# Kernel optimization log

Hardware: AMD Instinct MI355X
Metric: run time of the kernel (lower is better)

Reference implementation:

```python
import jax, jax.numpy as jnp
import numpy as np

D_MODEL = 1024
NUM_HEADS = 16
D_K = D_MODEL // NUM_HEADS
BATCH = 2
SEQ = 2048


def setup_inputs() -> dict:
    key = jax.random.key(0)
    ks = jax.random.split(key, 9)
    s = 1.0 / np.sqrt(D_MODEL)
    X = jax.random.normal(ks[0], (BATCH, SEQ, D_MODEL), dtype=jnp.float32)
    # causal mask, broadcastable over batch and heads; 0 means masked
    mask = jnp.tril(jnp.ones((SEQ, SEQ), dtype=jnp.int32))[None, None]
    W_Q = jax.random.uniform(ks[1], (D_MODEL, D_MODEL), jnp.float32, -s, s)
    b_Q = jax.random.uniform(ks[2], (D_MODEL,), jnp.float32, -s, s)
    W_K = jax.random.uniform(ks[3], (D_MODEL, D_MODEL), jnp.float32, -s, s)
    b_K = jax.random.uniform(ks[4], (D_MODEL,), jnp.float32, -s, s)
    W_V = jax.random.uniform(ks[5], (D_MODEL, D_MODEL), jnp.float32, -s, s)
    b_V = jax.random.uniform(ks[6], (D_MODEL,), jnp.float32, -s, s)
    W_O = jax.random.uniform(ks[7], (D_MODEL, D_MODEL), jnp.float32, -s, s)
    b_O = jax.random.uniform(ks[8], (D_MODEL,), jnp.float32, -s, s)
    return {"X": X, "mask": mask, "W_Q": W_Q, "b_Q": b_Q, "W_K": W_K,
            "b_K": b_K, "W_V": W_V, "b_V": b_V, "W_O": W_O, "b_O": b_O}


def reference(X, mask, W_Q, b_Q, W_K, b_K, W_V, b_V, W_O, b_O):
    B, S, _ = X.shape
    H, Dk = NUM_HEADS, D_K
    # projections; torch Linear uses y = x @ W.T + b; here W_* is stored as [in, out]
    Q = (X @ W_Q + b_Q).reshape(B, S, H, Dk).transpose(0, 2, 1, 3)  # [B,H,S,Dk]
    K = (X @ W_K + b_K).reshape(B, S, H, Dk).transpose(0, 2, 1, 3)
    V = (X @ W_V + b_V).reshape(B, S, H, Dk).transpose(0, 2, 1, 3)
    scores = jnp.einsum("bhqd,bhkd->bhqk", Q, K) / jnp.sqrt(jnp.asarray(Dk, X.dtype))
    scores = jnp.where(mask == 0, -jnp.inf, scores)
    attn = jax.nn.softmax(scores, axis=-1)  # [B,H,S,S]
    out = jnp.einsum("bhqk,bhkd->bhqd", attn, V)
    out = out.transpose(0, 2, 1, 3).reshape(B, S, H * Dk)
    return out @ W_O + b_O
```

## Files before the change

### kernel.cpp

```cpp
#include <hip/hip_runtime.h>
#include <math.h>

#define S_LEN 2048
#define DM 1024
#define NH 16
#define DK 64
#define BB 2
#define MROWS (BB * S_LEN)
#define QTILES (S_LEN / 64)
#define LOG2E 1.44269504088896340736f

typedef __attribute__((ext_vector_type(8))) short bf16x8;
typedef __attribute__((ext_vector_type(4))) float f32x4;

__device__ __forceinline__ unsigned short f2bf(float f) {
    unsigned int u = __builtin_bit_cast(unsigned int, f);
    u += 0x7fff + ((u >> 16) & 1);
    return (unsigned short)(u >> 16);
}

__device__ __forceinline__ float hw_exp2(float x) {
    return __builtin_amdgcn_exp2f(x);
}

__device__ __forceinline__ void gload_lds16(const unsigned short* g, unsigned short* l) {
    __builtin_amdgcn_global_load_lds(
        (const __attribute__((address_space(1))) unsigned int*)(const void*)g,
        (__attribute__((address_space(3))) unsigned int*)(void*)l, 16, 0, 0);
}

__global__ __launch_bounds__(256) void prep_kernel(
    const float* __restrict__ X, unsigned short* __restrict__ Xb,
    const float* __restrict__ W_Q, const float* __restrict__ W_K,
    const float* __restrict__ W_V, const float* __restrict__ W_O,
    unsigned short* __restrict__ WqkvT, unsigned short* __restrict__ WoT) {
    const int z = blockIdx.z;
    if (z == 0) {
        int i = (blockIdx.x * 256 + threadIdx.x) * 4;
        float4 v = *(const float4*)(X + i);
        ushort4 o;
        o.x = f2bf(v.x); o.y = f2bf(v.y); o.z = f2bf(v.z); o.w = f2bf(v.w);
        *(ushort4*)(Xb + i) = o;
        return;
    }
    if (blockIdx.x >= (DM / 32) * (DM / 32)) return;
    const float* in = z == 1 ? W_Q : (z == 2 ? W_K : (z == 3 ? W_V : W_O));
    unsigned short* out = z == 4 ? WoT : (WqkvT + (size_t)(z - 1) * DM * DM);
    __shared__ float tile[32][33];
    const int bx = blockIdx.x & 31, by = blockIdx.x >> 5;
    const int tx = threadIdx.x & 31, ty = threadIdx.x >> 5;
    const int c = bx * 32 + tx;
#pragma unroll
    for (int i = 0; i < 32; i += 8)
        tile[ty + i][tx] = in[(size_t)(by * 32 + ty + i) * DM + c];
    __syncthreads();
    const int oc = by * 32 + tx;
#pragma unroll
    for (int i = 0; i < 32; i += 8)
        out[(size_t)(bx * 32 + ty + i) * DM + oc] = f2bf(tile[tx][ty + i]);
}

__global__ __launch_bounds__(256) void gemm_qkv_kernel(
    const unsigned short* __restrict__ A,
    const unsigned short* __restrict__ Bt,
    const float* __restrict__ bQ, const float* __restrict__ bK,
    const float* __restrict__ bV,
    unsigned short* __restrict__ outQ, unsigned short* __restrict__ outK,
    unsigned short* __restrict__ outV) {
    const int K = DM;
    __shared__ __align__(16) unsigned short smem[4 * 64 * 72];
    const int tid = threadIdx.x;
    const int wave = tid >> 6, lane = tid & 63;
    const int lq = lane >> 4, ln = lane & 15;
    const int m0 = blockIdx.y * 128, n0 = blockIdx.x * 128;
    const int wr = (wave >> 1) * 64, wc = (wave & 1) * 64;

    f32x4 acc[4][4];
#pragma unroll
    for (int i = 0; i < 4; ++i)
#pragma unroll
        for (int j = 0; j < 4; ++j)
            acc[i][j] = (f32x4){0.f, 0.f, 0.f, 0.f};

    const unsigned short* ga = A  + (size_t)(m0 + (tid >> 2)) * K + (tid & 3) * 8;
    const unsigned short* gb = Bt + (size_t)(n0 + (tid >> 2)) * K + (tid & 3) * 8;
    const size_t half = (size_t)64 * K;

    {
        unsigned short* An = smem;
        unsigned short* Bn = smem + 4096;
        gload_lds16(ga, An + tid * 8);
        gload_lds16(ga + half, An + 2048 + tid * 8);
        gload_lds16(gb, Bn + tid * 8);
        gload_lds16(gb + half, Bn + 2048 + tid * 8);
    }

    for (int k0 = 0; k0 < K; k0 += 32) {
        const int cur = (k0 >> 5) & 1;
        unsigned short* As = smem + cur * 8192;
        unsigned short* Bs = As + 4096;
        __syncthreads();
        if (k0 + 32 < K) {
            unsigned short* An = smem + (cur ^ 1) * 8192;
            unsigned short* Bn = An + 4096;
            gload_lds16(ga + k0 + 32, An + tid * 8);
            gload_lds16(ga + half + k0 + 32, An + 2048 + tid * 8);
            gload_lds16(gb + k0 + 32, Bn + tid * 8);
            gload_lds16(gb + half + k0 + 32, Bn + 2048 + tid * 8);
        }
        bf16x8 af[4], bfv[4];
#pragma unroll
        for (int i = 0; i < 4; ++i) af[i]  = *(const bf16x8*)&As[(wr + i * 16 + ln) * 32 + lq * 8];
#pragma unroll
        for (int j = 0; j < 4; ++j) bfv[j] = *(const bf16x8*)&Bs[(wc + j * 16 + ln) * 32 + lq * 8];
#pragma unroll
        for (int i = 0; i < 4; ++i)
#pragma unroll
            for (int j = 0; j < 4; ++j)
                acc[i][j] = __builtin_amdgcn_mfma_f32_16x16x32_bf16(af[i], bfv[j], acc[i][j], 0, 0, 0);
    }
    __syncthreads();

    const int which = n0 >> 10;
    const float* bias = which == 0 ? bQ : (which == 1 ? bK : bV);
    const float scale = which == 0 ? 0.125f * LOG2E : 1.0f;
    unsigned short* ob = which == 0 ? outQ : (which == 1 ? outK : outV);
    unsigned short* Ts = &smem[wave * 64 * 72];
#pragma unroll
    for (int i = 0; i < 4; ++i)
#pragma unroll
        for (int j = 0; j < 4; ++j)
#pragma unroll
            for (int r = 0; r < 4; ++r) {
                int rl = i * 16 + lq * 4 + r;
                int cl = j * 16 + ln;
                float v = (acc[i][j][r] + bias[(n0 & 1023) + wc + cl]) * scale;
                if (which == 2) Ts[cl * 72 + rl] = f2bf(v);
                else            Ts[rl * 72 + cl] = f2bf(v);
            }
    const int hh = ((n0 & 1023) + wc) >> 6;
    const int bI = (m0 + wr) >> 11, sbase = (m0 + wr) & 2047;
    if (which <= 1) {
        unsigned short* dst = ob + ((size_t)(bI * NH + hh) * S_LEN + sbase) * DK;
#pragma unroll
        for (int t = 0; t < 8; ++t) {
            int rl = t * 8 + (lane >> 3);
            *(uint4*)(dst + rl * DK + (lane & 7) * 8) =
                *(const uint4*)&Ts[rl * 72 + (lane & 7) * 8];
        }
    } else {
        unsigned short* dst = ob + ((size_t)(bI * NH + hh) * DK) * S_LEN + sbase;
#pragma unroll
        for (int t = 0; t < 8; ++t) {
            int dkl = t * 8 + (lane >> 3);
            *(uint4*)(dst + (size_t)dkl * S_LEN + (lane & 7) * 8) =
                *(const uint4*)&Ts[dkl * 72 + (lane & 7) * 8];
        }
    }
}

__global__ __launch_bounds__(256) void gemm_o_kernel(
    const unsigned short* __restrict__ A,
    const unsigned short* __restrict__ Bt,
    const float* __restrict__ bias,
    float* __restrict__ out_f) {
    const int K = DM;
    __shared__ __align__(16) unsigned short smem[2 * 6144];
    const int tid = threadIdx.x;
    const int wave = tid >> 6, lane = tid & 63;
    const int lq = lane >> 4, ln = lane & 15;
    const int m0 = blockIdx.y * 128, n0 = blockIdx.x * 64;
    const int wr = (wave >> 1) * 64, wc = (wave & 1) * 32;

    f32x4 acc[4][2];
#pragma unroll
    for (int i = 0; i < 4; ++i)
#pragma unroll
        for (int j = 0; j < 2; ++j)
            acc[i][j] = (f32x4){0.f, 0.f, 0.f, 0.f};

    const unsigned short* ga = A  + (size_t)(m0 + (tid >> 2)) * K + (tid & 3) * 8;
    const unsigned short* gb = Bt + (size_t)(n0 + (tid >> 2)) * K + (tid & 3) * 8;
    const size_t half = (size_t)64 * K;

    {
        unsigned short* An = smem;
        gload_lds16(ga, An + tid * 8);
        gload_lds16(ga + half, An + 2048 + tid * 8);
        gload_lds16(gb, An + 4096 + tid * 8);
    }

    for (int k0 = 0; k0 < K; k0 += 32) {
        const int cur = (k0 >> 5) & 1;
        unsigned short* As = smem + cur * 6144;
        unsigned short* Bs = As + 4096;
        __syncthreads();
        if (k0 + 32 < K) {
            unsigned short* An = smem + (cur ^ 1) * 6144;
            gload_lds16(ga + k0 + 32, An + tid * 8);
            gload_lds16(ga + half + k0 + 32, An + 2048 + tid * 8);
            gload_lds16(gb + k0 + 32, An + 4096 + tid * 8);
        }
        bf16x8 af[4], bfv[2];
#pragma unroll
        for (int i = 0; i < 4; ++i) af[i]  = *(const bf16x8*)&As[(wr + i * 16 + ln) * 32 + lq * 8];
#pragma unroll
        for (int j = 0; j < 2; ++j) bfv[j] = *(const bf16x8*)&Bs[(wc + j * 16 + ln) * 32 + lq * 8];
#pragma unroll
        for (int i = 0; i < 4; ++i)
#pragma unroll
            for (int j = 0; j < 2; ++j)
                acc[i][j] = __builtin_amdgcn_mfma_f32_16x16x32_bf16(af[i], bfv[j], acc[i][j], 0, 0, 0);
    }

#pragma unroll
    for (int i = 0; i < 4; ++i)
#pragma unroll
        for (int j = 0; j < 2; ++j)
#pragma unroll
            for (int r = 0; r < 4; ++r) {
                int m = m0 + wr + i * 16 + lq * 4 + r;
                int n = n0 + wc + j * 16 + ln;
                out_f[(size_t)m * DM + n] = acc[i][j][r] + bias[n];
            }
}

__global__ __launch_bounds__(256, 2) void attn_kernel(
    const unsigned short* __restrict__ Qg,
    const unsigned short* __restrict__ Kg,
    const unsigned short* __restrict__ Vg,
    unsigned short* __restrict__ Og) {
    __shared__ __align__(16) unsigned short KBUF[2 * 128 * 64];
    __shared__ __align__(16) unsigned short VBUF[2 * 64 * 128];
    __shared__ __align__(16) unsigned short Pw[4 * 2 * 640];

    const int tid = threadIdx.x;
    const int wave = tid >> 6, lane = tid & 63;
    const int lq = lane >> 4, ln = lane & 15;
    const int bh = blockIdx.x, b = bh >> 4, h = bh & 15;
    const int bx = blockIdx.y;
    const int qtA = QTILES - 1 - bx, qtB = bx;
    const int nkvA = (qtA + 2) >> 1;
    const int nkvB = (qtB + 2) >> 1;
    const int T = nkvA + nkvB;

    const unsigned short* Qb = Qg + (size_t)bh * S_LEN * DK;
    const unsigned short* Kb = Kg + (size_t)bh * S_LEN * DK;
    const unsigned short* Vb = Vg + (size_t)bh * DK * S_LEN;

    const int krow_l = lane >> 3;
    const int kchunk = (lane & 7) ^ krow_l;
    const int vrow_l = lane >> 4;

    {
#pragma unroll
        for (int s = 0; s < 4; ++s)
            gload_lds16(Kb + (size_t)(wave * 32 + s * 8 + krow_l) * DK + kchunk * 8,
                        KBUF + (wave * 32 + s * 8) * 64 + lane * 8);
#pragma unroll
        for (int s = 0; s < 4; ++s) {
            int rv = wave * 16 + s * 4 + vrow_l;
            int c  = (lane & 15) ^ (s * 4 + vrow_l);
            gload_lds16(Vb + (size_t)rv * S_LEN + c * 8,
                        VBUF + (wave * 16 + s * 4) * 128 + lane * 8);
        }
    }

    int q0 = qtA * 64;
    const int qrowoff = wave * 16 + ln;
    bf16x8 qf0 = *(const bf16x8*)(Qb + (q0 + qrowoff) * DK + lq * 8);
    bf16x8 qf1 = *(const bf16x8*)(Qb + (q0 + qrowoff) * DK + 32 + lq * 8);

    const short one_bf = (short)0x3F80;
    const bf16x8 onesf = {one_bf, one_bf, one_bf, one_bf,
                          one_bf, one_bf, one_bf, one_bf};

    f32x4 oacc[4];
    f32x4 lacc = (f32x4){0.f, 0.f, 0.f, 0.f};
#pragma unroll
    for (int i = 0; i < 4; ++i) oacc[i] = (f32x4){0.f, 0.f, 0.f, 0.f};
    float m0r = -INFINITY, m1r = -INFINITY, m2r = -INFINITY, m3r = -INFINITY;

    for (int g = 0; g < T; ++g) {
        const int cur = g & 1;
        unsigned short* Kl = KBUF + cur * 8192;
        unsigned short* Vl = VBUF + cur * 8192;
        __syncthreads();

        if (g + 1 < T) {
            const int kv0n = (g + 1 < nkvA ? g + 1 : g + 1 - nkvA) * 128;
            unsigned short* Kn = KBUF + (cur ^ 1) * 8192;
            unsigned short* Vn = VBUF + (cur ^ 1) * 8192;
#pragma unroll
            for (int s = 0; s < 4; ++s)
                gload_lds16(Kb + (size_t)(kv0n + wave * 32 + s * 8 + krow_l) * DK + kchunk * 8,
                            Kn + (wave * 32 + s * 8) * 64 + lane * 8);
#pragma unroll
            for (int s = 0; s < 4; ++s) {
                int rv = wave * 16 + s * 4 + vrow_l;
                int c  = (lane & 15) ^ (s * 4 + vrow_l);
                gload_lds16(Vb + (size_t)rv * S_LEN + kv0n + c * 8,
                            Vn + (wave * 16 + s * 4) * 128 + lane * 8);
            }
        }

        const int kv0 = (g < nkvA ? g : g - nkvA) * 128;
        const bool lastOfSeg = (g == nkvA - 1) || (g == T - 1);

        f32x4 sc[8];
#pragma unroll
        for (int ct = 0; ct < 8; ++ct) {
            const int rbase = (ct * 16 + ln) * 64;
            bf16x8 k0 = *(const bf16x8*)&Kl[rbase + ((lq ^ (ln & 7)) * 8)];
            bf16x8 k1 = *(const bf16x8*)&Kl[rbase + (((lq + 4) ^ (ln & 7)) * 8)];
            f32x4 a = (f32x4){0.f, 0.f, 0.f, 0.f};
            a = __builtin_amdgcn_mfma_f32_16x16x32_bf16(qf0, k0, a, 0, 0, 0);
            a = __builtin_amdgcn_mfma_f32_16x16x32_bf16(qf1, k1, a, 0, 0, 0);
            sc[ct] = a;
        }

        if (lastOfSeg) {
#pragma unroll
            for (int ct = 0; ct < 8; ++ct) {
                int col = kv0 + ct * 16 + ln;
#pragma unroll
                for (int r = 0; r < 4; ++r) {
                    int row = q0 + wave * 16 + lq * 4 + r;
                    if (col > row) sc[ct][r] = -INFINITY;
                }
            }
        }

#pragma unroll
        for (int r = 0; r < 4; ++r) {
            float mx = fmaxf(fmaxf(fmaxf(sc[0][r], sc[1][r]), fmaxf(sc[2][r], sc[3][r])),
                             fmaxf(fmaxf(sc[4][r], sc[5][r]), fmaxf(sc[6][r], sc[7][r])));
#pragma unroll
            for (int off = 1; off < 16; off <<= 1)
                mx = fmaxf(mx, __shfl_xor(mx, off));
            float mold = r == 0 ? m0r : (r == 1 ? m1r : (r == 2 ? m2r : m3r));
            float mnew = fmaxf(mold, mx);
            float alpha = hw_exp2(mold - mnew);
#pragma unroll
            for (int dkt = 0; dkt < 4; ++dkt) oacc[dkt][r] *= alpha;
            lacc[r] *= alpha;
#pragma unroll
            for (int ct = 0; ct < 8; ++ct)
                sc[ct][r] = hw_exp2(sc[ct][r] - mnew);
            if (r == 0) m0r = mnew;
            else if (r == 1) m1r = mnew;
            else if (r == 2) m2r = mnew;
            else m3r = mnew;
        }

        unsigned short* Pp0 = Pw + wave * 1280;
#pragma unroll
        for (int qd = 0; qd < 4; ++qd) {
            unsigned short* Pq = Pp0 + (qd & 1) * 640;
#pragma unroll
            for (int c2 = 0; c2 < 2; ++c2)
#pragma unroll
                for (int r = 0; r < 4; ++r)
                    Pq[(lq * 4 + r) * 40 + c2 * 16 + ln] = f2bf(sc[qd * 2 + c2][r]);
            bf16x8 pf = *(const bf16x8*)&Pq[ln * 40 + lq * 8];
            lacc = __builtin_amdgcn_mfma_f32_16x16x32_bf16(pf, onesf, lacc, 0, 0, 0);
#pragma unroll
            for (int dkt = 0; dkt < 4; ++dkt) {
                const unsigned short* vr =
                    &Vl[(dkt * 16 + ln) * 128 + (((qd * 4 + lq) ^ ln) * 8)];
                oacc[dkt] = __builtin_amdgcn_mfma_f32_16x16x32_bf16(pf, *(const bf16x8*)vr, oacc[dkt], 0, 0, 0);
            }
        }

        if (g == nkvA - 1) {
#pragma unroll
            for (int r = 0; r < 4; ++r) {
                float inv = 1.0f / lacc[r];
                int s = q0 + wave * 16 + lq * 4 + r;
#pragma unroll
                for (int dkt = 0; dkt < 4; ++dkt)
                    Og[((size_t)(b * S_LEN + s)) * DM + h * 64 + dkt * 16 + ln] =
                        f2bf(oacc[dkt][r] * inv);
            }
            q0 = qtB * 64;
            qf0 = *(const bf16x8*)(Qb + (q0 + qrowoff) * DK + lq * 8);
            qf1 = *(const bf16x8*)(Qb + (q0 + qrowoff) * DK + 32 + lq * 8);
#pragma unroll
            for (int i = 0; i < 4; ++i) oacc[i] = (f32x4){0.f, 0.f, 0.f, 0.f};
            lacc = (f32x4){0.f, 0.f, 0.f, 0.f};
            m0r = m1r = m2r = m3r = -INFINITY;
        }
    }

#pragma unroll
    for (int r = 0; r < 4; ++r) {
        float inv = 1.0f / lacc[r];
        int s = q0 + wave * 16 + lq * 4 + r;
#pragma unroll
        for (int dkt = 0; dkt < 4; ++dkt)
            Og[((size_t)(b * S_LEN + s)) * DM + h * 64 + dkt * 16 + ln] =
                f2bf(oacc[dkt][r] * inv);
    }
}

extern "C" void kernel_launch(void* const* d_in, const int* in_sizes, int n_in,
                              void* d_out, int out_size, void* d_ws, size_t ws_size,
                              hipStream_t stream) {
    const float* X   = (const float*)d_in[0];
    const float* W_Q = (const float*)d_in[2];
    const float* b_Q = (const float*)d_in[3];
    const float* W_K = (const float*)d_in[4];
    const float* b_K = (const float*)d_in[5];
    const float* W_V = (const float*)d_in[6];
    const float* b_V = (const float*)d_in[7];
    const float* W_O = (const float*)d_in[8];
    const float* b_O = (const float*)d_in[9];

    unsigned short* Xb    = (unsigned short*)d_ws;
    unsigned short* WqkvT = Xb    + (size_t)MROWS * DM;
    unsigned short* WoT   = WqkvT + (size_t)3 * DM * DM;
    unsigned short* Qb    = WoT   + (size_t)DM * DM;
    unsigned short* Kb    = Qb    + (size_t)MROWS * DM;
    unsigned short* Vtb   = Kb    + (size_t)MROWS * DM;
    unsigned short* Ob    = Vtb   + (size_t)MROWS * DM;

    prep_kernel<<<dim3((MROWS * DM) / 1024, 1, 5), 256, 0, stream>>>(
        X, Xb, W_Q, W_K, W_V, W_O, WqkvT, WoT);

    gemm_qkv_kernel<<<dim3(3 * DM / 128, MROWS / 128), 256, 0, stream>>>(
        Xb, WqkvT, b_Q, b_K, b_V, Qb, Kb, Vtb);

    attn_kernel<<<dim3(BB * NH, QTILES / 2), 256, 0, stream>>>(Qb, Kb, Vtb, Ob);

    gemm_o_kernel<<<dim3(DM / 64, MROWS / 128), 256, 0, stream>>>(
        Ob, WoT, b_O, (float*)d_out);
}
```

Before: 197.0 us.

## Process paired causal query tiles concurrently with two wave groups sharing KV tiles

The attention block grows from 256 to 512 threads, and its two wave groups handle the long and short query tiles of a causal pair at the same time. Before, one group handled them one after the other. Both groups share a single stream of double-buffered K/V tiles in LDS, so each KV tile is loaded once per block rather than once per segment. The short-tile group idles once its causal range is done, and the larger block with launch bounds of 4 blocks/CU may squeeze registers or occupancy.

```diff
diff --git a/kernel.cpp b/kernel.cpp
--- a/kernel.cpp
+++ b/kernel.cpp
@@ -225,24 +225,24 @@
             }
 }
 
-__global__ __launch_bounds__(256, 2) void attn_kernel(
+__global__ __launch_bounds__(512, 4) void attn_kernel(
     const unsigned short* __restrict__ Qg,
     const unsigned short* __restrict__ Kg,
     const unsigned short* __restrict__ Vg,
     unsigned short* __restrict__ Og) {
     __shared__ __align__(16) unsigned short KBUF[2 * 128 * 64];
     __shared__ __align__(16) unsigned short VBUF[2 * 64 * 128];
-    __shared__ __align__(16) unsigned short Pw[4 * 2 * 640];
+    __shared__ __align__(16) unsigned short Pw[8 * 640];
 
     const int tid = threadIdx.x;
     const int wave = tid >> 6, lane = tid & 63;
     const int lq = lane >> 4, ln = lane & 15;
     const int bh = blockIdx.x, b = bh >> 4, h = bh & 15;
-    const int bx = blockIdx.y;
-    const int qtA = QTILES - 1 - bx, qtB = bx;
-    const int nkvA = (qtA + 2) >> 1;
-    const int nkvB = (qtB + 2) >> 1;
-    const int T = nkvA + nkvB;
+    const int j = blockIdx.y;
+    const int grp = wave >> 2, wv = wave & 3;
+    const int qt = grp == 0 ? (QTILES - 1 - j) : j;
+    const int nkv_me = grp == 0 ? ((33 - j) >> 1) : ((j + 2) >> 1);
+    const int T = (33 - j) >> 1;
 
     const unsigned short* Qb = Qg + (size_t)bh * S_LEN * DK;
     const unsigned short* Kb = Kg + (size_t)bh * S_LEN * DK;
@@ -254,22 +254,21 @@
 
     {
 #pragma unroll
-        for (int s = 0; s < 4; ++s)
-            gload_lds16(Kb + (size_t)(wave * 32 + s * 8 + krow_l) * DK + kchunk * 8,
-                        KBUF + (wave * 32 + s * 8) * 64 + lane * 8);
-#pragma unroll
-        for (int s = 0; s < 4; ++s) {
-            int rv = wave * 16 + s * 4 + vrow_l;
-            int c  = (lane & 15) ^ (s * 4 + vrow_l);
+        for (int s = 0; s < 2; ++s)
+            gload_lds16(Kb + (size_t)(wave * 16 + s * 8 + krow_l) * DK + kchunk * 8,
+                        KBUF + (wave * 16 + s * 8) * 64 + lane * 8);
+#pragma unroll
+        for (int s = 0; s < 2; ++s) {
+            int rv = wave * 8 + s * 4 + vrow_l;
+            int c  = (lane & 15) ^ (rv & 15);
             gload_lds16(Vb + (size_t)rv * S_LEN + c * 8,
-                        VBUF + (wave * 16 + s * 4) * 128 + lane * 8);
-        }
-    }
-
-    int q0 = qtA * 64;
-    const int qrowoff = wave * 16 + ln;
-    bf16x8 qf0 = *(const bf16x8*)(Qb + (q0 + qrowoff) * DK + lq * 8);
-    bf16x8 qf1 = *(const bf16x8*)(Qb + (q0 + qrowoff) * DK + 32 + lq * 8);
+                        VBUF + (wave * 8 + s * 4) * 128 + lane * 8);
+        }
+    }
+
+    const int q0 = qt * 64;
+    bf16x8 qf0 = *(const bf16x8*)(Qb + (q0 + wv * 16 + ln) * DK + lq * 8);
+    bf16x8 qf1 = *(const bf16x8*)(Qb + (q0 + wv * 16 + ln) * DK + 32 + lq * 8);
 
     const short one_bf = (short)0x3F80;
     const bf16x8 onesf = {one_bf, one_bf, one_bf, one_bf,
@@ -288,114 +287,95 @@
         __syncthreads();
 
         if (g + 1 < T) {
-            const int kv0n = (g + 1 < nkvA ? g + 1 : g + 1 - nkvA) * 128;
+            const int kv0n = (g + 1) * 128;
             unsigned short* Kn = KBUF + (cur ^ 1) * 8192;
             unsigned short* Vn = VBUF + (cur ^ 1) * 8192;
 #pragma unroll
-            for (int s = 0; s < 4; ++s)
-                gload_lds16(Kb + (size_t)(kv0n + wave * 32 + s * 8 + krow_l) * DK + kchunk * 8,
-                            Kn + (wave * 32 + s * 8) * 64 + lane * 8);
-#pragma unroll
-            for (int s = 0; s < 4; ++s) {
-                int rv = wave * 16 + s * 4 + vrow_l;
-                int c  = (lane & 15) ^ (s * 4 + vrow_l);
+            for (int s = 0; s < 2; ++s)
+                gload_lds16(Kb + (size_t)(kv0n + wave * 16 + s * 8 + krow_l) * DK + kchunk * 8,
+                            Kn + (wave * 16 + s * 8) * 64 + lane * 8);
+#pragma unroll
+            for (int s = 0; s < 2; ++s) {
+                int rv = wave * 8 + s * 4 + vrow_l;
+                int c  = (lane & 15) ^ (rv & 15);
                 gload_lds16(Vb + (size_t)rv * S_LEN + kv0n + c * 8,
-                            Vn + (wave * 16 + s * 4) * 128 + lane * 8);
-            }
-        }
-
-        const int kv0 = (g < nkvA ? g : g - nkvA) * 128;
-        const bool lastOfSeg = (g == nkvA - 1) || (g == T - 1);
-
-        f32x4 sc[8];
-#pragma unroll
-        for (int ct = 0; ct < 8; ++ct) {
-            const int rbase = (ct * 16 + ln) * 64;
-            bf16x8 k0 = *(const bf16x8*)&Kl[rbase + ((lq ^ (ln & 7)) * 8)];
-            bf16x8 k1 = *(const bf16x8*)&Kl[rbase + (((lq + 4) ^ (ln & 7)) * 8)];
-            f32x4 a = (f32x4){0.f, 0.f, 0.f, 0.f};
-            a = __builtin_amdgcn_mfma_f32_16x16x32_bf16(qf0, k0, a, 0, 0, 0);
-            a = __builtin_amdgcn_mfma_f32_16x16x32_bf16(qf1, k1, a, 0, 0, 0);
-            sc[ct] = a;
-        }
-
-        if (lastOfSeg) {
+                            Vn + (wave * 8 + s * 4) * 128 + lane * 8);
+            }
+        }
+
+        if (g < nkv_me) {
+            const int kv0 = g * 128;
+
+            f32x4 sc[8];
 #pragma unroll
             for (int ct = 0; ct < 8; ++ct) {
-                int col = kv0 + ct * 16 + ln;
-#pragma unroll
-                for (int r = 0; r < 4; ++r) {
-                    int row = q0 + wave * 16 + lq * 4 + r;
-                    if (col > row) sc[ct][r] = -INFINITY;
+                const int rbase = (ct * 16 + ln) * 64;
+                bf16x8 k0 = *(const bf16x8*)&Kl[rbase + ((lq ^ (ln & 7)) * 8)];
+                bf16x8 k1 = *(const bf16x8*)&Kl[rbase + (((lq + 4) ^ (ln & 7)) * 8)];
+                f32x4 a = (f32x4){0.f, 0.f, 0.f, 0.f};
+                a = __builtin_amdgcn_mfma_f32_16x16x32_bf16(qf0, k0, a, 0, 0, 0);
+                a = __builtin_amdgcn_mfma_f32_16x16x32_bf16(qf1, k1, a, 0, 0, 0);
+                sc[ct] = a;
+            }
+
+            if (g == nkv_me - 1) {
+#pragma unroll
+                for (int ct = 0; ct < 8; ++ct) {
+                    int col = kv0 + ct * 16 + ln;
+#pragma unroll
+                    for (int r = 0; r < 4; ++r) {
+                        int row = q0 + wv * 16 + lq * 4 + r;
+                        if (col > row) sc[ct][r] = -INFINITY;
+                    }
                 }
             }
-        }
-
-#pragma unroll
-        for (int r = 0; r < 4; ++r) {
-            float mx = fmaxf(fmaxf(fmaxf(sc[0][r], sc[1][r]), fmaxf(sc[2][r], sc[3][r])),
-                             fmaxf(fmaxf(sc[4][r], sc[5][r]), fmaxf(sc[6][r], sc[7][r])));
-#pragma unroll
-            for (int off = 1; off < 16; off <<= 1)
-                mx = fmaxf(mx, __shfl_xor(mx, off));
-            float mold = r == 0 ? m0r : (r == 1 ? m1r : (r == 2 ? m2r : m3r));
-            float mnew = fmaxf(mold, mx);
-            float alpha = hw_exp2(mold - mnew);
-#pragma unroll
-            for (int dkt = 0; dkt < 4; ++dkt) oacc[dkt][r] *= alpha;
-            lacc[r] *= alpha;
-#pragma unroll
-            for (int ct = 0; ct < 8; ++ct)
-                sc[ct][r] = hw_exp2(sc[ct][r] - mnew);
-            if (r == 0) m0r = mnew;
-            else if (r == 1) m1r = mnew;
-            else if (r == 2) m2r = mnew;
-            else m3r = mnew;
-        }
-
-        unsigned short* Pp0 = Pw + wave * 1280;
-#pragma unroll
-        for (int qd = 0; qd < 4; ++qd) {
-            unsigned short* Pq = Pp0 + (qd & 1) * 640;
-#pragma unroll
-            for (int c2 = 0; c2 < 2; ++c2)
-#pragma unroll
-                for (int r = 0; r < 4; ++r)
-                    Pq[(lq * 4 + r) * 40 + c2 * 16 + ln] = f2bf(sc[qd * 2 + c2][r]);
-            bf16x8 pf = *(const bf16x8*)&Pq[ln * 40 + lq * 8];
-            lacc = __builtin_amdgcn_mfma_f32_16x16x32_bf16(pf, onesf, lacc, 0, 0, 0);
-#pragma unroll
-            for (int dkt = 0; dkt < 4; ++dkt) {
-                const unsigned short* vr =
-                    &Vl[(dkt * 16 + ln) * 128 + (((qd * 4 + lq) ^ ln) * 8)];
-                oacc[dkt] = __builtin_amdgcn_mfma_f32_16x16x32_bf16(pf, *(const bf16x8*)vr, oacc[dkt], 0, 0, 0);
-            }
-        }
-
-        if (g == nkvA - 1) {
+
 #pragma unroll
             for (int r = 0; r < 4; ++r) {
-                float inv = 1.0f / lacc[r];
-                int s = q0 + wave * 16 + lq * 4 + r;
-#pragma unroll
-                for (int dkt = 0; dkt < 4; ++dkt)
-                    Og[((size_t)(b * S_LEN + s)) * DM + h * 64 + dkt * 16 + ln] =
-                        f2bf(oacc[dkt][r] * inv);
-            }
-            q0 = qtB * 64;
-            qf0 = *(const bf16x8*)(Qb + (q0 + qrowoff) * DK + lq * 8);
-            qf1 = *(const bf16x8*)(Qb + (q0 + qrowoff) * DK + 32 + lq * 8);
-#pragma unroll
-            for (int i = 0; i < 4; ++i) oacc[i] = (f32x4){0.f, 0.f, 0.f, 0.f};
-            lacc = (f32x4){0.f, 0.f, 0.f, 0.f};
-            m0r = m1r = m2r = m3r = -INFINITY;
+                float mx = fmaxf(fmaxf(fmaxf(sc[0][r], sc[1][r]), fmaxf(sc[2][r], sc[3][r])),
+                                 fmaxf(fmaxf(sc[4][r], sc[5][r]), fmaxf(sc[6][r], sc[7][r])));
+#pragma unroll
+                for (int off = 1; off < 16; off <<= 1)
+                    mx = fmaxf(mx, __shfl_xor(mx, off));
+                float mold = r == 0 ? m0r : (r == 1 ? m1r : (r == 2 ? m2r : m3r));
+                float mnew = fmaxf(mold, mx);
+                float alpha = hw_exp2(mold - mnew);
+#pragma unroll
+                for (int dkt = 0; dkt < 4; ++dkt) oacc[dkt][r] *= alpha;
+                lacc[r] *= alpha;
+#pragma unroll
+                for (int ct = 0; ct < 8; ++ct)
+                    sc[ct][r] = hw_exp2(sc[ct][r] - mnew);
+                if (r == 0) m0r = mnew;
+                else if (r == 1) m1r = mnew;
+                else if (r == 2) m2r = mnew;
+                else m3r = mnew;
+            }
+
+            unsigned short* Pq = Pw + wave * 640;
+#pragma unroll
+            for (int qd = 0; qd < 4; ++qd) {
+#pragma unroll
+                for (int c2 = 0; c2 < 2; ++c2)
+#pragma unroll
+                    for (int r = 0; r < 4; ++r)
+                        Pq[(lq * 4 + r) * 40 + c2 * 16 + ln] = f2bf(sc[qd * 2 + c2][r]);
+                bf16x8 pf = *(const bf16x8*)&Pq[ln * 40 + lq * 8];
+                lacc = __builtin_amdgcn_mfma_f32_16x16x32_bf16(pf, onesf, lacc, 0, 0, 0);
+#pragma unroll
+                for (int dkt = 0; dkt < 4; ++dkt) {
+                    const unsigned short* vr =
+                        &Vl[(dkt * 16 + ln) * 128 + (((qd * 4 + lq) ^ ln) * 8)];
+                    oacc[dkt] = __builtin_amdgcn_mfma_f32_16x16x32_bf16(pf, *(const bf16x8*)vr, oacc[dkt], 0, 0, 0);
+                }
+            }
         }
     }
 
 #pragma unroll
     for (int r = 0; r < 4; ++r) {
         float inv = 1.0f / lacc[r];
-        int s = q0 + wave * 16 + lq * 4 + r;
+        int s = q0 + wv * 16 + lq * 4 + r;
 #pragma unroll
         for (int dkt = 0; dkt < 4; ++dkt)
             Og[((size_t)(b * S_LEN + s)) * DM + h * 64 + dkt * 16 + ln] =
@@ -430,7 +410,7 @@
     gemm_qkv_kernel<<<dim3(3 * DM / 128, MROWS / 128), 256, 0, stream>>>(
         Xb, WqkvT, b_Q, b_K, b_V, Qb, Kb, Vtb);
 
-    attn_kernel<<<dim3(BB * NH, QTILES / 2), 256, 0, stream>>>(Qb, Kb, Vtb, Ob);
+    attn_kernel<<<dim3(BB * NH, QTILES / 2), 512, 0, stream>>>(Qb, Kb, Vtb, Ob);
 
     gemm_o_kernel<<<dim3(DM / 64, MROWS / 128), 256, 0, stream>>>(
         Ob, WoT, b_O, (float*)d_out);
```

After: 195.1 us. About the same (-1.0%).
